# Kernel optimization log

Hardware: AMD Instinct MI355X
Metric: run time of the kernel (lower is better)

Reference implementation:

```python
import jax, jax.numpy as jnp
import numpy as np

Q = 32          # latent position dim; state vs = [v, s] has dim 2Q
N = 131072      # batch of ODE states
H = 50          # BNN hidden width (n_hidden=50 in source)
STEPS = 16      # fixed-step Euler steps (dense time grid)
DT = 0.1        # dt default from forward()
LN_EPS = 1e-5


def setup_inputs() -> dict:
    key = jax.random.key(0)
    ks = jax.random.split(key, 6)
    d = 2 * Q
    # weights scaled by 1/sqrt(fan_in) so Euler integration stays stable
    return {
        "z0": jax.random.normal(ks[0], (N, d), jnp.float32),
        "logp0": jax.random.normal(ks[1], (N,), jnp.float32),
        "W1": jax.random.normal(ks[2], (d, H), jnp.float32) / np.sqrt(d).astype(np.float32),
        "b1": jnp.zeros((H,), jnp.float32),
        "g1": jnp.ones((H,), jnp.float32),
        "be1": jnp.zeros((H,), jnp.float32),
        "W2": jax.random.normal(ks[3], (H, H), jnp.float32) / np.sqrt(H).astype(np.float32),
        "b2": jnp.zeros((H,), jnp.float32),
        "g2": jnp.ones((H,), jnp.float32),
        "be2": jnp.zeros((H,), jnp.float32),
        "W3": jax.random.normal(ks[4], (H, Q), jnp.float32) / np.sqrt(H).astype(np.float32),
        "b3": jnp.zeros((Q,), jnp.float32),
    }


def _layernorm(x, g, b):
    m = jnp.mean(x, axis=-1, keepdims=True)
    v = jnp.mean((x - m) ** 2, axis=-1, keepdims=True)
    return (x - m) * jax.lax.rsqrt(v + LN_EPS) * g + b


def reference(z0, logp0, W1, b1, g1, be1, W2, b2, g2, be2, W3, b3):
    d = z0.shape[1]
    q = d // 2

    def f(vs):  # BNN dynamics: [N, 2q] -> [N, q]
        h = jax.nn.celu(_layernorm(vs @ W1 + b1, g1, be1))
        h = jax.nn.celu(_layernorm(h @ W2 + b2, g2, be2))
        return h @ W3 + b3

    basis = jnp.eye(q, d, dtype=z0.dtype)  # [q, 2q] unit tangents in the velocity block

    def rhs(vs):
        dv = f(vs)          # dv/dt = f(vs)
        ds = vs[:, :q]      # ds/dt = v
        dvs = jnp.concatenate([dv, ds], axis=1)
        # trace of d(dv)/d(v) via q forward-mode JVPs (fused analogue of the
        # per-dim torch.autograd.grad loop in ode2vae_rhs)
        def jvp_i(e):
            _, t = jax.jvp(f, (vs,), (jnp.broadcast_to(e, vs.shape),))
            return t  # [N, q]
        tang = jax.vmap(jvp_i)(basis)        # [q, N, q]
        tr = jnp.einsum("ini->n", tang)      # sum_i d(dv_i)/d(v_i)
        return dvs, -tr

    def step(carry, _):
        vs, lp = carry
        dvs, dlp = rhs(vs)
        vs2 = vs + DT * dvs
        lp2 = lp + DT * dlp
        return (vs2, lp2), (vs2, lp2)

    _, (zt, lp) = jax.lax.scan(step, (z0, logp0), None, length=STEPS)
    # [STEPS, N, 2q+1]: trajectory states with log-density appended
    return jnp.concatenate([zt, lp[..., None]], axis=-1)
```

## Files before the change

### kernel.cpp

```cpp
#include <hip/hip_runtime.h>
#include <hip/hip_fp16.h>

#define NPART 131072
#define QDIM 32
#define DDIM 64
#define HDIM 50
#define STEPS 16
#define DT 0.1f
#define LN_EPS 1e-5f
#define INV_H 0.02f
#define ODIM 65

#define WS_W1TH 0
#define WS_W2TH 1600
#define WS_UTH  3000
#define WS_MH   4400
#define WS_W3H  5800
#define WS_JV   6600
#define WS_HV   6800
#define WS_TOT  7000

#define LT_W1TH 0
#define LT_W2TH 1600
#define LT_UTH  3000
#define LT_TOT  4400

#define SLOT_FLOATS (HDIM * 256)
#define LDS_FLOATS  (SLOT_FLOATS + LT_TOT)

typedef float f4a __attribute__((ext_vector_type(4)));
typedef float f4u __attribute__((ext_vector_type(4), aligned(4)));
typedef unsigned int u32;
typedef _Float16 h2f __attribute__((ext_vector_type(2)));

__device__ __forceinline__ h2f as_h2(u32 x) { h2f r; __builtin_memcpy(&r, &x, 4); return r; }
__device__ __forceinline__ u32 h2bits(float a, float b) {
    h2f p; p[0] = (_Float16)a; p[1] = (_Float16)b;
    u32 r; __builtin_memcpy(&r, &p, 4); return r;
}
__device__ __forceinline__ h2f mk_h2(float a, float b) {
    h2f p; p[0] = (_Float16)a; p[1] = (_Float16)b; return p;
}

#if __has_builtin(__builtin_amdgcn_fdot2)
#define FDOT2(a, b, c) __builtin_amdgcn_fdot2((a), (b), (c), false)
#else
#define FDOT2(a, b, c) ((float)(a)[0] * (float)(b)[0] + ((float)(a)[1] * (float)(b)[1] + (c)))
#endif

__device__ __forceinline__ float pack2h(float x, float t) {
    u32 r = h2bits(x, t); float f; __builtin_memcpy(&f, &r, 4); return f;
}
__device__ __forceinline__ void unpack2h(float f, float& x, float& t) {
    u32 u; __builtin_memcpy(&u, &f, 4); h2f p = as_h2(u); x = (float)p[0]; t = (float)p[1];
}

__global__ void ode2vae_setup(const float* __restrict__ W1,
                              const float* __restrict__ W2,
                              const float* __restrict__ W3,
                              const float* __restrict__ b1, const float* __restrict__ g1,
                              const float* __restrict__ be1,
                              const float* __restrict__ b2, const float* __restrict__ g2,
                              const float* __restrict__ be2,
                              float* __restrict__ ws)
{
    const int tid = threadIdx.x;
    u32* wsu = (u32*)ws;
    for (int i = tid; i < WS_TOT; i += 256) wsu[i] = 0u;
    __syncthreads();
    for (int idx = tid; idx < HDIM * 32; idx += 256) {
        const int h = idx / 32, k = idx % 32;
        wsu[WS_W1TH + h * 32 + k] = h2bits(W1[(2 * k) * HDIM + h], W1[(2 * k + 1) * HDIM + h]);
    }
    for (int idx = tid; idx < HDIM * 25; idx += 256) {
        const int j = idx / 25, k = idx % 25;
        float w2p[2], up[2], mp[2];
        #pragma unroll
        for (int s_ = 0; s_ < 2; ++s_) {
            const int h = 2 * k + s_;
            float u = 0.f;
            #pragma unroll
            for (int i = 0; i < QDIM; ++i)
                u = fmaf(W1[i * HDIM + h], W3[j * QDIM + i], u);
            const float w2 = W2[h * HDIM + j];
            float rs = 0.f;
            for (int jj = 0; jj < HDIM; ++jj) rs += W2[h * HDIM + jj];
            w2p[s_] = w2; up[s_] = u; mp[s_] = u * (w2 - INV_H * rs);
        }
        wsu[WS_W2TH + j * 28 + k] = h2bits(w2p[0], w2p[1]);
        wsu[WS_UTH  + j * 28 + k] = h2bits(up[0], up[1]);
        wsu[WS_MH   + j * 28 + k] = h2bits(mp[0], mp[1]);
    }
    for (int idx = tid; idx < HDIM * 16; idx += 256) {
        const int j = idx / 16, k = idx % 16;
        wsu[WS_W3H + j * 16 + k] = h2bits(W3[j * QDIM + 2 * k], W3[j * QDIM + 2 * k + 1]);
    }
    if (tid < HDIM) {
        float acc = 0.f;
        #pragma unroll
        for (int i = 0; i < QDIM; ++i) {
            float rs1 = 0.f;
            for (int h = 0; h < HDIM; ++h) rs1 += W1[i * HDIM + h];
            acc = fmaf(rs1, W3[tid * QDIM + i], acc);
        }
        ws[WS_JV + tid * 4 + 0] = g2[tid];
        ws[WS_JV + tid * 4 + 1] = be2[tid];
        ws[WS_JV + tid * 4 + 2] = b2[tid];
        ws[WS_JV + tid * 4 + 3] = acc;
        ws[WS_HV + tid * 4 + 0] = b1[tid];
        ws[WS_HV + tid * 4 + 1] = g1[tid];
        ws[WS_HV + tid * 4 + 2] = be1[tid];
        ws[WS_HV + tid * 4 + 3] = 0.f;
    }
}

#define DOT64(res, rowp, P)                                           \
    {                                                                 \
        float q0 = 0.f, q1 = 0.f, q2 = 0.f, q3 = 0.f;                 \
        const uint4* R_ = (const uint4*)(rowp);                       \
        _Pragma("unroll")                                             \
        for (int c_ = 0; c_ < 8; ++c_) {                              \
            const uint4 u_ = R_[c_];                                  \
            q0 = FDOT2(as_h2(u_.x), (P)[4*c_ + 0], q0);               \
            q1 = FDOT2(as_h2(u_.y), (P)[4*c_ + 1], q1);               \
            q2 = FDOT2(as_h2(u_.z), (P)[4*c_ + 2], q2);               \
            q3 = FDOT2(as_h2(u_.w), (P)[4*c_ + 3], q3);               \
        }                                                             \
        res = (q0 + q1) + (q2 + q3);                                  \
    }
#define DOT56(res, rowp, P)                                           \
    {                                                                 \
        float q0 = 0.f, q1 = 0.f, q2 = 0.f, q3 = 0.f;                 \
        const uint4* R_ = (const uint4*)(rowp);                       \
        _Pragma("unroll")                                             \
        for (int c_ = 0; c_ < 7; ++c_) {                              \
            const uint4 u_ = R_[c_];                                  \
            q0 = FDOT2(as_h2(u_.x), (P)[4*c_ + 0], q0);               \
            q1 = FDOT2(as_h2(u_.y), (P)[4*c_ + 1], q1);               \
            q2 = FDOT2(as_h2(u_.z), (P)[4*c_ + 2], q2);               \
            q3 = FDOT2(as_h2(u_.w), (P)[4*c_ + 3], q3);               \
        }                                                             \
        res = (q0 + q1) + (q2 + q3);                                  \
    }

#define LDROW7(RB, SRC) { const uint4* S_ = (const uint4*)(SRC);      \
    _Pragma("unroll") for (int c_ = 0; c_ < 7; ++c_) RB[c_] = S_[c_]; }
#define LDROW4(RB, SRC) { const uint4* S_ = (const uint4*)(SRC);      \
    _Pragma("unroll") for (int c_ = 0; c_ < 4; ++c_) RB[c_] = S_[c_]; }

#define PKDOT_RB(res, RB, P)                                          \
    {                                                                 \
        h2f a0 = mk_h2(0.f, 0.f), a1_ = a0;                           \
        _Pragma("unroll")                                             \
        for (int c_ = 0; c_ < 7; ++c_) {                              \
            a0  = as_h2(RB[c_].x) * (P)[4*c_ + 0] + a0;               \
            a1_ = as_h2(RB[c_].y) * (P)[4*c_ + 1] + a1_;              \
            a0  = as_h2(RB[c_].z) * (P)[4*c_ + 2] + a0;               \
            a1_ = as_h2(RB[c_].w) * (P)[4*c_ + 3] + a1_;              \
        }                                                             \
        a0 = a0 + a1_;                                                \
        res = (float)a0[0] + (float)a0[1];                            \
    }

#define PK3DOT_RB(rA, rB, rC, RB, PA, PB, PC)                         \
    {                                                                 \
        h2f aA = mk_h2(0.f, 0.f), aB = aA, aC = aA;                   \
        _Pragma("unroll")                                             \
        for (int c_ = 0; c_ < 7; ++c_) {                              \
            const h2f x_ = as_h2(RB[c_].x), y_ = as_h2(RB[c_].y);     \
            const h2f z_ = as_h2(RB[c_].z), w_ = as_h2(RB[c_].w);     \
            aA = x_ * (PA)[4*c_ + 0] + aA;                            \
            aB = x_ * (PB)[4*c_ + 0] + aB;                            \
            aC = x_ * (PC)[4*c_ + 0] + aC;                            \
            aA = y_ * (PA)[4*c_ + 1] + aA;                            \
            aB = y_ * (PB)[4*c_ + 1] + aB;                            \
            aC = y_ * (PC)[4*c_ + 1] + aC;                            \
            aA = z_ * (PA)[4*c_ + 2] + aA;                            \
            aB = z_ * (PB)[4*c_ + 2] + aB;                            \
            aC = z_ * (PC)[4*c_ + 2] + aC;                            \
            aA = w_ * (PA)[4*c_ + 3] + aA;                            \
            aB = w_ * (PB)[4*c_ + 3] + aB;                            \
            aC = w_ * (PC)[4*c_ + 3] + aC;                            \
        }                                                             \
        rA = (float)aA[0] + (float)aA[1];                             \
        rB = (float)aB[0] + (float)aB[1];                             \
        rC = (float)aC[0] + (float)aC[1];                             \
    }

#define SAXPY_RB7(RB, sh, D)                                          \
    {                                                                 \
        _Pragma("unroll")                                             \
        for (int c_ = 0; c_ < 7; ++c_) {                              \
            (D)[4*c_ + 0] = as_h2(RB[c_].x) * (sh) + (D)[4*c_ + 0];   \
            (D)[4*c_ + 1] = as_h2(RB[c_].y) * (sh) + (D)[4*c_ + 1];   \
            (D)[4*c_ + 2] = as_h2(RB[c_].z) * (sh) + (D)[4*c_ + 2];   \
            (D)[4*c_ + 3] = as_h2(RB[c_].w) * (sh) + (D)[4*c_ + 3];   \
        }                                                             \
    }
#define SAXPY_RB4(RB, sh, D)                                          \
    {                                                                 \
        _Pragma("unroll")                                             \
        for (int c_ = 0; c_ < 4; ++c_) {                              \
            (D)[4*c_ + 0] = as_h2(RB[c_].x) * (sh) + (D)[4*c_ + 0];   \
            (D)[4*c_ + 1] = as_h2(RB[c_].y) * (sh) + (D)[4*c_ + 1];   \
            (D)[4*c_ + 2] = as_h2(RB[c_].z) * (sh) + (D)[4*c_ + 2];   \
            (D)[4*c_ + 3] = as_h2(RB[c_].w) * (sh) + (D)[4*c_ + 3];   \
        }                                                             \
    }

__global__ __launch_bounds__(256, 2)
void ode2vae_main(const float* __restrict__ z0, const float* __restrict__ logp0,
                  const float* __restrict__ b3,
                  const float* __restrict__ wsc,
                  float* out)
{
    __shared__ float lds[LDS_FLOATS];
    const int tid = threadIdx.x;
    const int n = blockIdx.x * 256 + tid;

    {
        const u32* src = (const u32*)wsc;
        u32* dst = (u32*)(lds + SLOT_FLOATS);
        for (int i = tid; i < 1600; i += 256) dst[LT_W1TH + i] = src[WS_W1TH + i];
        for (int i = tid; i < 1400; i += 256) dst[LT_W2TH + i] = src[WS_W2TH + i];
        for (int i = tid; i < 1400; i += 256) dst[LT_UTH + i]  = src[WS_UTH + i];
    }
    __syncthreads();

    float* const L = lds + tid;
    const u32* LW1TH = (const u32*)(lds + SLOT_FLOATS) + LT_W1TH;
    const u32* LW2TH = (const u32*)(lds + SLOT_FLOATS) + LT_W2TH;
    const u32* LUTH  = (const u32*)(lds + SLOT_FLOATS) + LT_UTH;
    const u32* GMH   = (const u32*)wsc + WS_MH;
    const u32* GW3H  = (const u32*)wsc + WS_W3H;
    const f4a* GJV   = (const f4a*)(wsc + WS_JV);
    const f4a* GHV   = (const f4a*)(wsc + WS_HV);

    float zq[QDIM];
    {
        const f4a* zp = (const f4a*)(z0 + (size_t)n * DDIM);
        #pragma unroll
        for (int k = 0; k < 8; ++k) {
            f4a v = zp[k];
            zq[4*k] = v[0]; zq[4*k+1] = v[1]; zq[4*k+2] = v[2]; zq[4*k+3] = v[3];
        }
    }
    float lp = logp0[n];

    for (int s = 0; s < STEPS; ++s) {
        float* const odst = out + ((size_t)s * NPART + (size_t)n) * ODIM;
        const float* const zsprev = (s == 0)
            ? (z0 + (size_t)n * DDIM + QDIM)
            : (out + ((size_t)(s - 1) * NPART + (size_t)n) * ODIM + QDIM);

        float zs[QDIM];
        #pragma unroll
        for (int k = 0; k < 8; ++k) {
            f4u v = *(const f4u*)(zsprev + 4 * k);
            zs[4*k] = v[0]; zs[4*k+1] = v[1]; zs[4*k+2] = v[2]; zs[4*k+3] = v[3];
        }
        h2f zp[32];
        #pragma unroll
        for (int k = 0; k < 16; ++k) zp[k] = mk_h2(zq[2*k], zq[2*k+1]);
        #pragma unroll
        for (int k = 0; k < 16; ++k) zp[16 + k] = mk_h2(zs[2*k], zs[2*k+1]);

        float m1a = 0.f, v1a = 0.f;
        #pragma unroll 1
        for (int h = 0; h < HDIM; ++h) {
            float a1h;
            DOT64(a1h, LW1TH + h * 32, zp);
            const f4a hv = GHV[h];
            a1h += hv[0];
            L[h * 256] = a1h;
            m1a += a1h;
            v1a = fmaf(a1h, a1h, v1a);
        }
        #pragma unroll
        for (int k = 0; k < QDIM; ++k) zs[k] = fmaf(DT, zq[k], zs[k]);
        #pragma unroll
        for (int k = 0; k < 8; ++k) {
            f4u v = {zs[4*k], zs[4*k+1], zs[4*k+2], zs[4*k+3]};
            *(f4u*)(odst + QDIM + 4 * k) = v;
        }
        const float m1 = m1a * INV_H;
        float var1 = v1a * INV_H - m1 * m1;
        var1 = var1 > 0.f ? var1 : 0.f;
        const float r1 = rsqrtf(var1 + LN_EPS);

        h2f xh1p[28], hhp[28], w1vp[28], w1xp[28];
        #pragma unroll
        for (int hp = 0; hp < 25; ++hp) {
            const float xa = (L[(2*hp) * 256] - m1) * r1;
            const float xb = (L[(2*hp + 1) * 256] - m1) * r1;
            const f4a hva = GHV[2*hp], hvb = GHV[2*hp + 1];
            const float ya = fmaf(xa, hva[1], hva[2]);
            const float yb = fmaf(xb, hvb[1], hvb[2]);
            const float ea = __expf(ya), eb = __expf(yb);
            const float ca = (ya > 0.f) ? ya : (ea - 1.f);
            const float cb = (yb > 0.f) ? yb : (eb - 1.f);
            const float wa = ((ya > 0.f) ? 1.f : ea) * (hva[1] * r1);
            const float wb = ((yb > 0.f) ? 1.f : eb) * (hvb[1] * r1);
            xh1p[hp] = mk_h2(xa, xb);
            hhp[hp]  = mk_h2(ca, cb);
            w1vp[hp] = mk_h2(wa, wb);
            w1xp[hp] = mk_h2(wa * xa, wb * xb);
        }
        #pragma unroll
        for (int hp = 25; hp < 28; ++hp) {
            xh1p[hp] = mk_h2(0.f, 0.f); hhp[hp] = mk_h2(0.f, 0.f);
            w1vp[hp] = mk_h2(0.f, 0.f); w1xp[hp] = mk_h2(0.f, 0.f);
        }

        float m2a = 0.f, v2a = 0.f;
        #pragma unroll 1
        for (int j = 0; j < HDIM; ++j) {
            float a2j;
            DOT56(a2j, LW2TH + j * 28, hhp);
            const f4a jv = GJV[j];
            a2j += jv[2];
            L[j * 256] = a2j;
            m2a += a2j;
            v2a = fmaf(a2j, a2j, v2a);
        }
        const float m2 = m2a * INV_H;
        float var2 = v2a * INV_H - m2 * m2;
        var2 = var2 > 0.f ? var2 : 0.f;
        const float r2 = rsqrtf(var2 + LN_EPS);

        h2f duyp[28];
        #pragma unroll
        for (int k = 0; k < 28; ++k) duyp[k] = mk_h2(0.f, 0.f);
        float suA = 0.f, syA = 0.f, tuA = 0.f, tyA = 0.f;
        #pragma unroll 1
        for (int j = 0; j < HDIM; ++j) {
            uint4 RB[7];
            LDROW7(RB, LUTH + j * 28);
            const float x2 = (L[j * 256] - m2) * r2;
            const f4a jv = GJV[j];
            const float y = fmaf(x2, jv[0], jv[1]);
            const float e = __expf(y);
            const float w2vj = ((y > 0.f) ? 1.f : e) * (jv[0] * r2);
            float t;
            PKDOT_RB(t, RB, xh1p);
            const float tw = w2vj * t;
            const float y3 = x2 * w2vj;
            const h2f y3h = mk_h2(y3, y3);
            SAXPY_RB7(RB, y3h, duyp);
            L[j * 256] = pack2h(x2, tw);
            tuA += tw; tyA = fmaf(tw, x2, tyA);
            const float sw = jv[3] * w2vj;
            suA += sw; syA = fmaf(sw, x2, syA);
        }
        const float suH = suA * INV_H, syH = syA * INV_H;
        const float tuH = tuA * INV_H, tyH = tyA * INV_H;

        #pragma unroll
        for (int k = 0; k < 28; ++k) duyp[k] = duyp[k] * w1vp[k];

        float S2 = 0.f, S3 = 0.f, T1c = 0.f, T1A = 0.f;
        h2f dvp[16];
        #pragma unroll
        for (int k = 0; k < 16; ++k) dvp[k] = mk_h2(0.f, 0.f);
        #pragma unroll 1
        for (int j = 0; j < HDIM; ++j) {
            uint4 RC[7];
            LDROW7(RC, GMH + j * 28);
            uint4 RB4[4];
            LDROW4(RB4, GW3H + j * 16);
            float x2, tw; unpack2h(L[j * 256], x2, tw);
            const f4a jv = GJV[j];
            const float y = fmaf(x2, jv[0], jv[1]);
            const float e = __expf(y);
            const float w2vj = ((y > 0.f) ? 1.f : e) * (jv[0] * r2);
            const float h2v = (y > 0.f) ? y : (e - 1.f);
            const float q1 = fmaf(-syH, x2, jv[3] * w2vj - suH);
            const float q2 = fmaf(-tyH, x2, tw - tuH);
            uint4 RB[7];
            LDROW7(RB, LW2TH + j * 28);
            float cS2, cS3, cTc;
            PK3DOT_RB(cS2, cS3, cTc, RB, w1vp, w1xp, duyp);
            float cTA;
            PKDOT_RB(cTA, RC, w1vp);
            const h2f hb = mk_h2(h2v, h2v);
            SAXPY_RB4(RB4, hb, dvp);
            S2  = fmaf(q1, cS2, S2);
            S3  = fmaf(q2, cS3, S3);
            T1c = fmaf(x2, cTc, T1c);
            T1A = fmaf(w2vj, cTA, T1A);
        }
        const float tr = T1A - (T1c + S2 + S3) * INV_H;

        lp = fmaf(-DT, tr, lp);
        #pragma unroll
        for (int k = 0; k < 16; ++k) {
            const float da = (float)dvp[k][0] + b3[2*k];
            const float db = (float)dvp[k][1] + b3[2*k + 1];
            zq[2*k]     = fmaf(DT, da, zq[2*k]);
            zq[2*k + 1] = fmaf(DT, db, zq[2*k + 1]);
        }
        #pragma unroll
        for (int k = 0; k < 8; ++k) {
            f4u v = {zq[4*k], zq[4*k+1], zq[4*k+2], zq[4*k+3]};
            *(f4u*)(odst + 4 * k) = v;
        }
        odst[DDIM] = lp;
    }
}

extern "C" void kernel_launch(void* const* d_in, const int* in_sizes, int n_in,
                              void* d_out, int out_size, void* d_ws, size_t ws_size,
                              hipStream_t stream)
{
    const float* z0    = (const float*)d_in[0];
    const float* logp0 = (const float*)d_in[1];
    const float* W1    = (const float*)d_in[2];
    const float* b1    = (const float*)d_in[3];
    const float* g1    = (const float*)d_in[4];
    const float* be1   = (const float*)d_in[5];
    const float* W2    = (const float*)d_in[6];
    const float* b2    = (const float*)d_in[7];
    const float* g2    = (const float*)d_in[8];
    const float* be2   = (const float*)d_in[9];
    const float* W3    = (const float*)d_in[10];
    const float* b3    = (const float*)d_in[11];
    float* out = (float*)d_out;
    float* ws  = (float*)d_ws;

    hipLaunchKernelGGL(ode2vae_setup, dim3(1), dim3(256), 0, stream,
                       W1, W2, W3, b1, g1, be1, b2, g2, be2, ws);
    hipLaunchKernelGGL(ode2vae_main, dim3(NPART / 256), dim3(256), 0, stream,
                       z0, logp0, b3, ws, out);
}
```

Measured before the change: 1.377 ms.

## Fuse two hidden-layer trace loops into one pass via algebraic expansion

Merges the two per-step loops over hidden units into a single loop. The q1/q2 weighting terms, which depend on the full-row sums su/sy/tu/ty, are expanded algebraically into separate accumulators that are combined after the loop. The duyp-weighted W2 dot is replaced by accumulating a second packed vector php and taking one final dot product. To reduce register pressure, W1 now comes from global memory instead of LDS, and the velocity state is re-read from the previous output row rather than kept in registers. The aim is to cut redundant exp/LDS traffic and the pack/unpack of intermediates, at the cost of more global/L2 loads and a different fp16 accumulation order.

Result: faster. 1.347 ms (-2.2%).

```diff
diff --git a/kernel.cpp b/kernel.cpp
--- a/kernel.cpp
+++ b/kernel.cpp
@@ -20,10 +20,9 @@
 #define WS_HV   6800
 #define WS_TOT  7000
 
-#define LT_W1TH 0
-#define LT_W2TH 1600
-#define LT_UTH  3000
-#define LT_TOT  4400
+#define LT_W2TH 0
+#define LT_UTH  1400
+#define LT_TOT  2800
 
 #define SLOT_FLOATS (HDIM * 256)
 #define LDS_FLOATS  (SLOT_FLOATS + LT_TOT)
@@ -47,13 +46,6 @@
 #else
 #define FDOT2(a, b, c) ((float)(a)[0] * (float)(b)[0] + ((float)(a)[1] * (float)(b)[1] + (c)))
 #endif
-
-__device__ __forceinline__ float pack2h(float x, float t) {
-    u32 r = h2bits(x, t); float f; __builtin_memcpy(&f, &r, 4); return f;
-}
-__device__ __forceinline__ void unpack2h(float f, float& x, float& t) {
-    u32 u; __builtin_memcpy(&u, &f, 4); h2f p = as_h2(u); x = (float)p[0]; t = (float)p[1];
-}
 
 __global__ void ode2vae_setup(const float* __restrict__ W1,
                               const float* __restrict__ W2,
@@ -162,41 +154,50 @@
         res = (float)a0[0] + (float)a0[1];                            \
     }
 
-#define PK3DOT_RB(rA, rB, rC, RB, PA, PB, PC)                         \
-    {                                                                 \
-        h2f aA = mk_h2(0.f, 0.f), aB = aA, aC = aA;                   \
+#define PKDOT_SAX_RB(res, RB, PA, ys, D)                              \
+    {                                                                 \
+        h2f a0 = mk_h2(0.f, 0.f), a1_ = a0;                           \
+        _Pragma("unroll")                                             \
+        for (int c_ = 0; c_ < 7; ++c_) {                              \
+            const h2f x_ = as_h2(RB[c_].x), y_ = as_h2(RB[c_].y);     \
+            const h2f z_ = as_h2(RB[c_].z), w_ = as_h2(RB[c_].w);     \
+            a0  = x_ * (PA)[4*c_ + 0] + a0;                           \
+            (D)[4*c_ + 0] = x_ * (ys) + (D)[4*c_ + 0];                \
+            a1_ = y_ * (PA)[4*c_ + 1] + a1_;                          \
+            (D)[4*c_ + 1] = y_ * (ys) + (D)[4*c_ + 1];                \
+            a0  = z_ * (PA)[4*c_ + 2] + a0;                           \
+            (D)[4*c_ + 2] = z_ * (ys) + (D)[4*c_ + 2];                \
+            a1_ = w_ * (PA)[4*c_ + 3] + a1_;                          \
+            (D)[4*c_ + 3] = w_ * (ys) + (D)[4*c_ + 3];                \
+        }                                                             \
+        a0 = a0 + a1_;                                                \
+        res = (float)a0[0] + (float)a0[1];                            \
+    }
+
+#define PK2DOT_SAX_RB(rA, rB, RB, PA, PB, xs, D)                      \
+    {                                                                 \
+        h2f aA = mk_h2(0.f, 0.f), aB = aA;                            \
         _Pragma("unroll")                                             \
         for (int c_ = 0; c_ < 7; ++c_) {                              \
             const h2f x_ = as_h2(RB[c_].x), y_ = as_h2(RB[c_].y);     \
             const h2f z_ = as_h2(RB[c_].z), w_ = as_h2(RB[c_].w);     \
             aA = x_ * (PA)[4*c_ + 0] + aA;                            \
             aB = x_ * (PB)[4*c_ + 0] + aB;                            \
-            aC = x_ * (PC)[4*c_ + 0] + aC;                            \
+            (D)[4*c_ + 0] = x_ * (xs) + (D)[4*c_ + 0];                \
             aA = y_ * (PA)[4*c_ + 1] + aA;                            \
             aB = y_ * (PB)[4*c_ + 1] + aB;                            \
-            aC = y_ * (PC)[4*c_ + 1] + aC;                            \
+            (D)[4*c_ + 1] = y_ * (xs) + (D)[4*c_ + 1];                \
             aA = z_ * (PA)[4*c_ + 2] + aA;                            \
             aB = z_ * (PB)[4*c_ + 2] + aB;                            \
-            aC = z_ * (PC)[4*c_ + 2] + aC;                            \
+            (D)[4*c_ + 2] = z_ * (xs) + (D)[4*c_ + 2];                \
             aA = w_ * (PA)[4*c_ + 3] + aA;                            \
             aB = w_ * (PB)[4*c_ + 3] + aB;                            \
-            aC = w_ * (PC)[4*c_ + 3] + aC;                            \
+            (D)[4*c_ + 3] = w_ * (xs) + (D)[4*c_ + 3];                \
         }                                                             \
         rA = (float)aA[0] + (float)aA[1];                             \
         rB = (float)aB[0] + (float)aB[1];                             \
-        rC = (float)aC[0] + (float)aC[1];                             \
-    }
-
-#define SAXPY_RB7(RB, sh, D)                                          \
-    {                                                                 \
-        _Pragma("unroll")                                             \
-        for (int c_ = 0; c_ < 7; ++c_) {                              \
-            (D)[4*c_ + 0] = as_h2(RB[c_].x) * (sh) + (D)[4*c_ + 0];   \
-            (D)[4*c_ + 1] = as_h2(RB[c_].y) * (sh) + (D)[4*c_ + 1];   \
-            (D)[4*c_ + 2] = as_h2(RB[c_].z) * (sh) + (D)[4*c_ + 2];   \
-            (D)[4*c_ + 3] = as_h2(RB[c_].w) * (sh) + (D)[4*c_ + 3];   \
-        }                                                             \
-    }
+    }
+
 #define SAXPY_RB4(RB, sh, D)                                          \
     {                                                                 \
         _Pragma("unroll")                                             \
@@ -221,42 +222,37 @@
     {
         const u32* src = (const u32*)wsc;
         u32* dst = (u32*)(lds + SLOT_FLOATS);
-        for (int i = tid; i < 1600; i += 256) dst[LT_W1TH + i] = src[WS_W1TH + i];
         for (int i = tid; i < 1400; i += 256) dst[LT_W2TH + i] = src[WS_W2TH + i];
         for (int i = tid; i < 1400; i += 256) dst[LT_UTH + i]  = src[WS_UTH + i];
     }
     __syncthreads();
 
     float* const L = lds + tid;
-    const u32* LW1TH = (const u32*)(lds + SLOT_FLOATS) + LT_W1TH;
     const u32* LW2TH = (const u32*)(lds + SLOT_FLOATS) + LT_W2TH;
     const u32* LUTH  = (const u32*)(lds + SLOT_FLOATS) + LT_UTH;
+    const u32* GW1TH = (const u32*)wsc + WS_W1TH;
     const u32* GMH   = (const u32*)wsc + WS_MH;
     const u32* GW3H  = (const u32*)wsc + WS_W3H;
     const f4a* GJV   = (const f4a*)(wsc + WS_JV);
     const f4a* GHV   = (const f4a*)(wsc + WS_HV);
 
-    float zq[QDIM];
-    {
-        const f4a* zp = (const f4a*)(z0 + (size_t)n * DDIM);
-        #pragma unroll
-        for (int k = 0; k < 8; ++k) {
-            f4a v = zp[k];
-            zq[4*k] = v[0]; zq[4*k+1] = v[1]; zq[4*k+2] = v[2]; zq[4*k+3] = v[3];
-        }
-    }
     float lp = logp0[n];
+    const float* const zrow0 = z0 + (size_t)n * DDIM;
 
     for (int s = 0; s < STEPS; ++s) {
         float* const odst = out + ((size_t)s * NPART + (size_t)n) * ODIM;
-        const float* const zsprev = (s == 0)
-            ? (z0 + (size_t)n * DDIM + QDIM)
-            : (out + ((size_t)(s - 1) * NPART + (size_t)n) * ODIM + QDIM);
-
-        float zs[QDIM];
+        const float* const zprev = (s == 0) ? zrow0
+            : (out + ((size_t)(s - 1) * NPART + (size_t)n) * ODIM);
+
+        float zq[QDIM], zs[QDIM];
         #pragma unroll
         for (int k = 0; k < 8; ++k) {
-            f4u v = *(const f4u*)(zsprev + 4 * k);
+            f4u v = *(const f4u*)(zprev + 4 * k);
+            zq[4*k] = v[0]; zq[4*k+1] = v[1]; zq[4*k+2] = v[2]; zq[4*k+3] = v[3];
+        }
+        #pragma unroll
+        for (int k = 0; k < 8; ++k) {
+            f4u v = *(const f4u*)(zprev + QDIM + 4 * k);
             zs[4*k] = v[0]; zs[4*k+1] = v[1]; zs[4*k+2] = v[2]; zs[4*k+3] = v[3];
         }
         h2f zp[32];
@@ -269,7 +265,7 @@
         #pragma unroll 1
         for (int h = 0; h < HDIM; ++h) {
             float a1h;
-            DOT64(a1h, LW1TH + h * 32, zp);
+            DOT64(a1h, GW1TH + h * 32, zp);
             const f4a hv = GHV[h];
             a1h += hv[0];
             L[h * 256] = a1h;
@@ -328,66 +324,78 @@
         var2 = var2 > 0.f ? var2 : 0.f;
         const float r2 = rsqrtf(var2 + LN_EPS);
 
-        h2f duyp[28];
-        #pragma unroll
-        for (int k = 0; k < 28; ++k) duyp[k] = mk_h2(0.f, 0.f);
+        h2f duyp[28], php[28];
+        #pragma unroll
+        for (int k = 0; k < 28; ++k) { duyp[k] = mk_h2(0.f, 0.f); php[k] = mk_h2(0.f, 0.f); }
+        h2f dvp[16];
+        #pragma unroll
+        for (int k = 0; k < 16; ++k) dvp[k] = mk_h2(0.f, 0.f);
         float suA = 0.f, syA = 0.f, tuA = 0.f, tyA = 0.f;
+        float A2a = 0.f, A2b = 0.f, A2c = 0.f;
+        float A3a = 0.f, A3b = 0.f, A3c = 0.f;
+        float T1A = 0.f;
         #pragma unroll 1
         for (int j = 0; j < HDIM; ++j) {
-            uint4 RB[7];
-            LDROW7(RB, LUTH + j * 28);
             const float x2 = (L[j * 256] - m2) * r2;
             const f4a jv = GJV[j];
             const float y = fmaf(x2, jv[0], jv[1]);
             const float e = __expf(y);
             const float w2vj = ((y > 0.f) ? 1.f : e) * (jv[0] * r2);
-            float t;
-            PKDOT_RB(t, RB, xh1p);
-            const float tw = w2vj * t;
+            const float h2v = (y > 0.f) ? y : (e - 1.f);
+
+            uint4 RU[7];
+            LDROW7(RU, LUTH + j * 28);
             const float y3 = x2 * w2vj;
             const h2f y3h = mk_h2(y3, y3);
-            SAXPY_RB7(RB, y3h, duyp);
-            L[j * 256] = pack2h(x2, tw);
-            tuA += tw; tyA = fmaf(tw, x2, tyA);
-            const float sw = jv[3] * w2vj;
-            suA += sw; syA = fmaf(sw, x2, syA);
-        }
+            float t;
+            PKDOT_SAX_RB(t, RU, xh1p, y3h, duyp);
+
+            uint4 RW[7];
+            LDROW7(RW, LW2TH + j * 28);
+            const h2f x2h = mk_h2(x2, x2);
+            float cS2, cS3;
+            PK2DOT_SAX_RB(cS2, cS3, RW, w1vp, w1xp, x2h, php);
+
+            uint4 RM[7];
+            LDROW7(RM, GMH + j * 28);
+            float cTA;
+            PKDOT_RB(cTA, RM, w1vp);
+
+            uint4 R3[4];
+            LDROW4(R3, GW3H + j * 16);
+            const h2f hb = mk_h2(h2v, h2v);
+            SAXPY_RB4(R3, hb, dvp);
+
+            const float svw = jv[3] * w2vj;
+            const float tw  = w2vj * t;
+            suA += svw; syA = fmaf(svw, x2, syA);
+            tuA += tw;  tyA = fmaf(tw, x2, tyA);
+            A2a = fmaf(svw, cS2, A2a); A2b += cS2; A2c = fmaf(x2, cS2, A2c);
+            A3a = fmaf(tw,  cS3, A3a); A3b += cS3; A3c = fmaf(x2, cS3, A3c);
+            T1A = fmaf(w2vj, cTA, T1A);
+        }
+
+        float zq2[QDIM];
+        #pragma unroll
+        for (int k = 0; k < 8; ++k) {
+            f4u v = *(const f4u*)(zprev + 4 * k);
+            zq2[4*k] = v[0]; zq2[4*k+1] = v[1]; zq2[4*k+2] = v[2]; zq2[4*k+3] = v[3];
+        }
+
         const float suH = suA * INV_H, syH = syA * INV_H;
         const float tuH = tuA * INV_H, tyH = tyA * INV_H;
-
-        #pragma unroll
-        for (int k = 0; k < 28; ++k) duyp[k] = duyp[k] * w1vp[k];
-
-        float S2 = 0.f, S3 = 0.f, T1c = 0.f, T1A = 0.f;
-        h2f dvp[16];
-        #pragma unroll
-        for (int k = 0; k < 16; ++k) dvp[k] = mk_h2(0.f, 0.f);
-        #pragma unroll 1
-        for (int j = 0; j < HDIM; ++j) {
-            uint4 RC[7];
-            LDROW7(RC, GMH + j * 28);
-            uint4 RB4[4];
-            LDROW4(RB4, GW3H + j * 16);
-            float x2, tw; unpack2h(L[j * 256], x2, tw);
-            const f4a jv = GJV[j];
-            const float y = fmaf(x2, jv[0], jv[1]);
-            const float e = __expf(y);
-            const float w2vj = ((y > 0.f) ? 1.f : e) * (jv[0] * r2);
-            const float h2v = (y > 0.f) ? y : (e - 1.f);
-            const float q1 = fmaf(-syH, x2, jv[3] * w2vj - suH);
-            const float q2 = fmaf(-tyH, x2, tw - tuH);
-            uint4 RB[7];
-            LDROW7(RB, LW2TH + j * 28);
-            float cS2, cS3, cTc;
-            PK3DOT_RB(cS2, cS3, cTc, RB, w1vp, w1xp, duyp);
-            float cTA;
-            PKDOT_RB(cTA, RC, w1vp);
-            const h2f hb = mk_h2(h2v, h2v);
-            SAXPY_RB4(RB4, hb, dvp);
-            S2  = fmaf(q1, cS2, S2);
-            S3  = fmaf(q2, cS3, S3);
-            T1c = fmaf(x2, cTc, T1c);
-            T1A = fmaf(w2vj, cTA, T1A);
+        const float S2 = A2a - suH * A2b - syH * A2c;
+        const float S3 = A3a - tuH * A3b - tyH * A3c;
+        float T1c;
+        {
+            h2f acc0 = mk_h2(0.f, 0.f), acc1 = acc0;
+            #pragma unroll
+            for (int k = 0; k < 28; k += 2) {
+                acc0 = (w1vp[k] * duyp[k]) * php[k] + acc0;
+                acc1 = (w1vp[k+1] * duyp[k+1]) * php[k+1] + acc1;
+            }
+            acc0 = acc0 + acc1;
+            T1c = (float)acc0[0] + (float)acc0[1];
         }
         const float tr = T1A - (T1c + S2 + S3) * INV_H;
 
@@ -396,12 +404,12 @@
         for (int k = 0; k < 16; ++k) {
             const float da = (float)dvp[k][0] + b3[2*k];
             const float db = (float)dvp[k][1] + b3[2*k + 1];
-            zq[2*k]     = fmaf(DT, da, zq[2*k]);
-            zq[2*k + 1] = fmaf(DT, db, zq[2*k + 1]);
+            zq2[2*k]     = fmaf(DT, da, zq2[2*k]);
+            zq2[2*k + 1] = fmaf(DT, db, zq2[2*k + 1]);
         }
         #pragma unroll
         for (int k = 0; k < 8; ++k) {
-            f4u v = {zq[4*k], zq[4*k+1], zq[4*k+2], zq[4*k+3]};
+            f4u v = {zq2[4*k], zq2[4*k+1], zq2[4*k+2], zq2[4*k+3]};
             *(f4u*)(odst + 4 * k) = v;
         }
         odst[DDIM] = lp;
```
